# Kernel optimization log

Hardware: AMD Instinct MI355X
Metric: run time of the kernel (lower is better)

Reference implementation:

```python
import jax, jax.numpy as jnp
import numpy as np

B, N, D = 4, 256, 128
HID = 128
IN_DIM = 4 * D + 4  # h_i, h_j, |h_i-h_j|, h_i*h_j + 2 base + 2 completion feats


def setup_inputs() -> dict:
    key = jax.random.key(0)
    k1, k2, k3, k4, k5, k6, k7 = jax.random.split(key, 7)
    node_latents = jax.random.normal(k1, (B, N, D), dtype=jnp.float32)
    base_edge_logits = jax.random.normal(k2, (B, N, N), dtype=jnp.float32)
    completion_logits = jax.random.normal(k3, (B, N, N), dtype=jnp.float32)
    # MLP params (build_mlp: Linear(in,hid) -> ReLU -> Linear(hid,1) for num_layers=2)
    s1 = 1.0 / np.sqrt(IN_DIM)
    s2 = 1.0 / np.sqrt(HID)
    W1 = jax.random.uniform(k4, (IN_DIM, HID), minval=-s1, maxval=s1, dtype=jnp.float32)
    b1 = jax.random.uniform(k5, (HID,), minval=-s1, maxval=s1, dtype=jnp.float32)
    W2 = jax.random.uniform(k6, (HID, 1), minval=-s2, maxval=s2, dtype=jnp.float32)
    b2 = jax.random.uniform(k7, (1,), minval=-s2, maxval=s2, dtype=jnp.float32)
    return {"node_latents": node_latents, "base_edge_logits": base_edge_logits,
            "completion_logits": completion_logits, "W1": W1, "b1": b1, "W2": W2, "b2": b2}


def reference(node_latents, base_edge_logits, completion_logits, W1, b1, W2, b2):
    bsz, num_nodes, hidden_dim = node_latents.shape
    h_i = jnp.broadcast_to(node_latents[:, :, None, :], (bsz, num_nodes, num_nodes, hidden_dim))
    h_j = jnp.broadcast_to(node_latents[:, None, :, :], (bsz, num_nodes, num_nodes, hidden_dim))
    base = jnp.clip(base_edge_logits, -20.0, 20.0)
    comp = jnp.clip(completion_logits, -20.0, 20.0)
    pair_feat = jnp.concatenate([
        h_i, h_j, jnp.abs(h_i - h_j), h_i * h_j,
        base[..., None], jax.nn.sigmoid(base)[..., None],
        comp[..., None], jax.nn.sigmoid(comp)[..., None],
    ], axis=-1)  # [B, N, N, IN_DIM]
    hdn = jax.nn.relu(jnp.einsum('bijf,fh->bijh', pair_feat, W1) + b1)
    logits = (jnp.einsum('bijh,ho->bijo', hdn, W2) + b2)[..., 0]  # [B, N, N]
    logits = 0.5 * (logits + jnp.swapaxes(logits, 1, 2))
    diag = jnp.eye(num_nodes, dtype=bool)[None]
    return jnp.where(diag, jnp.float32(-1e9), logits)
```

## Files before the change

kernel.cpp:

```cpp
#include <hip/hip_runtime.h>
#include <cstdint>


typedef float f32x4 __attribute__((ext_vector_type(4)));

#define INV256 0.00390625f

__device__ __forceinline__ uint32_t pk4(float a, float b, float c, float d) {
  uint32_t u = __builtin_amdgcn_cvt_pk_fp8_f32(a, b, 0, false);
  u = __builtin_amdgcn_cvt_pk_fp8_f32(c, d, u, true);
  return u;
}
__device__ __forceinline__ float bf2f(unsigned short u) {
  uint32_t x = ((uint32_t)u) << 16;
  return __builtin_bit_cast(float, x);
}
__device__ __forceinline__ long mk64(uint32_t lo, uint32_t hi) {
  return (long)((((unsigned long long)hi) << 32) | lo);
}

__global__ __launch_bounds__(128) void pre_k(const float* __restrict__ node,
                                             const float* __restrict__ W1,
                                             const float* __restrict__ b1,
                                             float* __restrict__ PiB,
                                             unsigned short* __restrict__ Pjh,
                                             uint32_t* __restrict__ W1f8,
                                             float* __restrict__ out) {
  int bid = blockIdx.x;
  int tid = threadIdx.x;
  if (bid < 32) {
    int ks = bid >> 2, nip = (bid >> 1) & 1, wn = bid & 1;
    int lane = tid & 63, nilow = tid >> 6;
    int quad = lane >> 4, col = lane & 15;
    int h = wn * 64 + (nip * 2 + nilow) * 16 + col;
    int k0 = ks * 32 + quad * 8;
    float w[8];
#pragma unroll
    for (int t = 0; t < 8; ++t) w[t] = W1[(256 + k0 + t) * 128 + h] * 256.0f;
    uint2 u;
    u.x = pk4(w[0], w[1], w[2], w[3]);
    u.y = pk4(w[4], w[5], w[6], w[7]);
    reinterpret_cast<uint2*>(W1f8)[(bid * 64 + lane) * 2 + nilow] = u;
  } else if (bid < 1056) {
    __shared__ float sN[128];
    int row = bid - 32;
    int h = tid;
    sN[h] = node[row * 128 + h];
    __syncthreads();
    float ai = 0.f, aj = 0.f;
#pragma unroll 8
    for (int d = 0; d < 128; ++d) {
      float v = sN[d];
      ai = fmaf(v, W1[d * 128 + h], ai);
      aj = fmaf(v, W1[(128 + d) * 128 + h], aj);
    }
    PiB[row * 128 + h] = ai + b1[h];
    Pjh[row * 128 + h] = (unsigned short)(__builtin_bit_cast(uint32_t, aj) >> 16);
  } else {
    int r = bid - 1056;
    int i = r & 255;
    out[r * 256 + tid] = (tid == i) ? -1e9f : 0.0f;
    out[r * 256 + 128 + tid] = (tid + 128 == i) ? -1e9f : 0.0f;
  }
}

__global__ __launch_bounds__(256, 3) void main_k(
    const float* __restrict__ node, const float* __restrict__ baseL,
    const float* __restrict__ compL, const float* __restrict__ W1,
    const float* __restrict__ W2, const float* __restrict__ b2,
    const uint32_t* __restrict__ W1f8, const float* __restrict__ PiB,
    const unsigned short* __restrict__ Pjh, float* __restrict__ out) {
  __shared__ __align__(16) char smem[16640 + 32768];
  __shared__ float sHi[128];
  __shared__ float sScal[64][4];
  char* sF = smem;
  char* sB = smem + 16640;

  const int tid = threadIdx.x;
  const int bx = blockIdx.x;
  const int jt = bx & 3;
  const int i = (bx >> 2) & 255;
  const int b = bx >> 10;
  const int j0 = jt * 64;
  const int rowI = b * 256 + i;
  const int jbase = b * 256 + j0;

  const int lane = tid & 63;
  const int wave = tid >> 6;
  const int wm = wave >> 1, wn = wave & 1;
  const int col = lane & 15, quad = lane >> 4;

  uint4 g[8];
#pragma unroll
  for (int it = 0; it < 8; ++it)
    g[it] = reinterpret_cast<const uint4*>(W1f8)[it * 256 + tid];

  float pj[2][4][4];
#pragma unroll
  for (int mi = 0; mi < 2; ++mi)
#pragma unroll
    for (int r = 0; r < 4; ++r) {
      int p = wm * 32 + mi * 16 + quad * 4 + r;
      const unsigned short* row = Pjh + (size_t)(jbase + p) * 128 + wn * 64 + col;
#pragma unroll
      for (int ni = 0; ni < 4; ++ni) pj[mi][r][ni] = bf2f(row[ni * 16]);
    }

  float cCi[4], cW2[4], cB0[4], cB1[4], cB2[4], cB3[4];
#pragma unroll
  for (int ni = 0; ni < 4; ++ni) {
    int h = wn * 64 + ni * 16 + col;
    cCi[ni] = PiB[rowI * 128 + h];
    cW2[ni] = W2[h];
    cB0[ni] = W1[512 * 128 + h];
    cB1[ni] = W1[513 * 128 + h];
    cB2[ni] = W1[514 * 128 + h];
    cB3[ni] = W1[515 * 128 + h];
  }
  const float b2v = b2[0];

  if (tid < 128) sHi[tid] = node[rowI * 128 + tid];
  if (tid < 64) {
    float bl = fminf(fmaxf(baseL[rowI * 256 + j0 + tid], -20.f), 20.f);
    float cl = fminf(fmaxf(compL[rowI * 256 + j0 + tid], -20.f), 20.f);
    sScal[tid][0] = bl;
    sScal[tid][1] = 1.f / (1.f + __expf(-bl));
    sScal[tid][2] = cl;
    sScal[tid][3] = 1.f / (1.f + __expf(-cl));
  }
#pragma unroll
  for (int it = 0; it < 8; ++it)
    reinterpret_cast<uint4*>(sB)[it * 256 + tid] = g[it];
  __syncthreads();

  {
    const int d4 = tid & 31;
    const int r = tid >> 5;
    const float4 hi = *reinterpret_cast<const float4*>(&sHi[d4 * 4]);
    const int ks1 = d4 >> 3;
    const int qj = (d4 >> 1) & 3;
    const int kb = (d4 & 1) * 4;
#pragma unroll
    for (int pass = 0; pass < 8; ++pass) {
      int j = pass * 8 + r;
      const float4 hj =
          *reinterpret_cast<const float4*>(node + (size_t)(jbase + j) * 128 + d4 * 4);
      uint32_t du = pk4(fabsf(hi.x - hj.x), fabsf(hi.y - hj.y),
                        fabsf(hi.z - hj.z), fabsf(hi.w - hj.w));
      uint32_t pu = pk4(hi.x * hj.x, hi.y * hj.y, hi.z * hj.z, hi.w * hj.w);
      int colj = j & 15, m16 = j >> 4;
      int off = (m16 >> 1) * 1024 + (qj * 16 + colj) * 16 + (m16 & 1) * 8 + kb;
      *reinterpret_cast<uint32_t*>(sF + ks1 * 2080 + off) = du;
      *reinterpret_cast<uint32_t*>(sF + (4 + ks1) * 2080 + off) = pu;
    }
  }
  __syncthreads();

  f32x4 acc[2][4] = {};
#pragma unroll
  for (int ks = 0; ks < 8; ++ks) {
    uint4 b01 = *reinterpret_cast<const uint4*>(sB + ((ks * 2 + 0) * 2 + wn) * 1024 + lane * 16);
    uint4 b23 = *reinterpret_cast<const uint4*>(sB + ((ks * 2 + 1) * 2 + wn) * 1024 + lane * 16);
    uint4 aa = *reinterpret_cast<const uint4*>(sF + ks * 2080 + wm * 1024 + lane * 16);
    long a0 = mk64(aa.x, aa.y), a1 = mk64(aa.z, aa.w);
    long bb0 = mk64(b01.x, b01.y), bb1 = mk64(b01.z, b01.w);
    long bb2 = mk64(b23.x, b23.y), bb3 = mk64(b23.z, b23.w);
    acc[0][0] = __builtin_amdgcn_mfma_f32_16x16x32_fp8_fp8(a0, bb0, acc[0][0], 0, 0, 0);
    acc[0][1] = __builtin_amdgcn_mfma_f32_16x16x32_fp8_fp8(a0, bb1, acc[0][1], 0, 0, 0);
    acc[0][2] = __builtin_amdgcn_mfma_f32_16x16x32_fp8_fp8(a0, bb2, acc[0][2], 0, 0, 0);
    acc[0][3] = __builtin_amdgcn_mfma_f32_16x16x32_fp8_fp8(a0, bb3, acc[0][3], 0, 0, 0);
    acc[1][0] = __builtin_amdgcn_mfma_f32_16x16x32_fp8_fp8(a1, bb0, acc[1][0], 0, 0, 0);
    acc[1][1] = __builtin_amdgcn_mfma_f32_16x16x32_fp8_fp8(a1, bb1, acc[1][1], 0, 0, 0);
    acc[1][2] = __builtin_amdgcn_mfma_f32_16x16x32_fp8_fp8(a1, bb2, acc[1][2], 0, 0, 0);
    acc[1][3] = __builtin_amdgcn_mfma_f32_16x16x32_fp8_fp8(a1, bb3, acc[1][3], 0, 0, 0);
  }

  __syncthreads();
  float(*sPart)[33] = reinterpret_cast<float(*)[33]>(sF);

#pragma unroll
  for (int mi = 0; mi < 2; ++mi) {
#pragma unroll
    for (int r = 0; r < 4; ++r) {
      int p = wm * 32 + mi * 16 + quad * 4 + r;
      float s0 = sScal[p][0], s1 = sScal[p][1], s2 = sScal[p][2], s3 = sScal[p][3];
      float val = 0.f;
#pragma unroll
      for (int ni = 0; ni < 4; ++ni) {
        float pre = fmaf(acc[mi][ni][r], INV256, cCi[ni]) + pj[mi][r][ni];
        pre = fmaf(s0, cB0[ni], pre);
        pre = fmaf(s1, cB1[ni], pre);
        pre = fmaf(s2, cB2[ni], pre);
        pre = fmaf(s3, cB3[ni], pre);
        val = fmaf(fmaxf(pre, 0.f), cW2[ni], val);
      }
      sPart[p][wn * 16 + col] = val;
    }
  }
  __syncthreads();
  if (tid < 64) {
    float s = b2v;
#pragma unroll
    for (int c = 0; c < 32; ++c) s += sPart[tid][c];
    int jg = j0 + tid;
    if (jg != i) {
      atomicAdd(out + (size_t)(b * 256 + i) * 256 + jg, 0.5f * s);
      atomicAdd(out + (size_t)(b * 256 + jg) * 256 + i, 0.5f * s);
    }
  }
}

extern "C" void kernel_launch(void* const* d_in, const int* in_sizes, int n_in,
                              void* d_out, int out_size, void* d_ws, size_t ws_size,
                              hipStream_t stream) {
  const float* node = (const float*)d_in[0];
  const float* baseL = (const float*)d_in[1];
  const float* compL = (const float*)d_in[2];
  const float* W1 = (const float*)d_in[3];
  const float* b1 = (const float*)d_in[4];
  const float* W2 = (const float*)d_in[5];
  const float* b2 = (const float*)d_in[6];
  float* out = (float*)d_out;

  char* ws = (char*)d_ws;
  float* PiB = (float*)(ws);
  unsigned short* Pjh = (unsigned short*)(ws + (512 << 10));
  uint32_t* W1f8 = (uint32_t*)(ws + (768 << 10));

  pre_k<<<2080, 128, 0, stream>>>(node, W1, b1, PiB, Pjh, W1f8, out);
  main_k<<<4096, 256, 0, stream>>>(node, baseL, compL, W1, W2, b2, W1f8, PiB, Pjh, out);
}
```

Measured before the change: 105.3 us.

## Exploit pair symmetry: compute upper-triangular 8x8 tiles, write both orders directly

```diff
diff --git a/kernel.cpp b/kernel.cpp
--- a/kernel.cpp
+++ b/kernel.cpp
@@ -11,10 +11,6 @@
   u = __builtin_amdgcn_cvt_pk_fp8_f32(c, d, u, true);
   return u;
 }
-__device__ __forceinline__ float bf2f(unsigned short u) {
-  uint32_t x = ((uint32_t)u) << 16;
-  return __builtin_bit_cast(float, x);
-}
 __device__ __forceinline__ long mk64(uint32_t lo, uint32_t hi) {
   return (long)((((unsigned long long)hi) << 32) | lo);
 }
@@ -23,9 +19,8 @@
                                              const float* __restrict__ W1,
                                              const float* __restrict__ b1,
                                              float* __restrict__ PiB,
-                                             unsigned short* __restrict__ Pjh,
-                                             uint32_t* __restrict__ W1f8,
-                                             float* __restrict__ out) {
+                                             float* __restrict__ Pjf,
+                                             uint32_t* __restrict__ W1f8) {
   int bid = blockIdx.x;
   int tid = threadIdx.x;
   if (bid < 32) {
@@ -41,7 +36,7 @@
     u.x = pk4(w[0], w[1], w[2], w[3]);
     u.y = pk4(w[4], w[5], w[6], w[7]);
     reinterpret_cast<uint2*>(W1f8)[(bid * 64 + lane) * 2 + nilow] = u;
-  } else if (bid < 1056) {
+  } else {
     __shared__ float sN[128];
     int row = bid - 32;
     int h = tid;
@@ -55,12 +50,7 @@
       aj = fmaf(v, W1[(128 + d) * 128 + h], aj);
     }
     PiB[row * 128 + h] = ai + b1[h];
-    Pjh[row * 128 + h] = (unsigned short)(__builtin_bit_cast(uint32_t, aj) >> 16);
-  } else {
-    int r = bid - 1056;
-    int i = r & 255;
-    out[r * 256 + tid] = (tid == i) ? -1e9f : 0.0f;
-    out[r * 256 + 128 + tid] = (tid + 128 == i) ? -1e9f : 0.0f;
+    Pjf[row * 128 + h] = aj;
   }
 }
 
@@ -69,21 +59,25 @@
     const float* __restrict__ compL, const float* __restrict__ W1,
     const float* __restrict__ W2, const float* __restrict__ b2,
     const uint32_t* __restrict__ W1f8, const float* __restrict__ PiB,
-    const unsigned short* __restrict__ Pjh, float* __restrict__ out) {
+    const float* __restrict__ Pjf, float* __restrict__ out) {
   __shared__ __align__(16) char smem[16640 + 32768];
-  __shared__ float sHi[128];
-  __shared__ float sScal[64][4];
+  __shared__ float sScalF[64][4];
+  __shared__ float sScalM[64][4];
   char* sF = smem;
   char* sB = smem + 16640;
+  float* sNode = reinterpret_cast<float*>(sB);
 
   const int tid = threadIdx.x;
   const int bx = blockIdx.x;
-  const int jt = bx & 3;
-  const int i = (bx >> 2) & 255;
-  const int b = bx >> 10;
-  const int j0 = jt * 64;
-  const int rowI = b * 256 + i;
-  const int jbase = b * 256 + j0;
+  const int b = bx / 528;
+  const int t = bx - b * 528;
+  int tI = (int)((65.0f - sqrtf(4225.0f - 8.0f * (float)t)) * 0.5f);
+  tI = (tI < 0) ? 0 : (tI > 31 ? 31 : tI);
+  while (((65 * tI - tI * tI) >> 1) > t) --tI;
+  while (tI < 31 && ((65 * (tI + 1) - (tI + 1) * (tI + 1)) >> 1) <= t) ++tI;
+  const int tJ = tI + (t - ((65 * tI - tI * tI) >> 1));
+  const int I0 = tI * 8, J0 = tJ * 8;
+  const int rowB = b * 256;
 
   const int lane = tid & 63;
   const int wave = tid >> 6;
@@ -95,22 +89,33 @@
   for (int it = 0; it < 8; ++it)
     g[it] = reinterpret_cast<const uint4*>(W1f8)[it * 256 + tid];
 
-  float pj[2][4][4];
-#pragma unroll
-  for (int mi = 0; mi < 2; ++mi)
-#pragma unroll
-    for (int r = 0; r < 4; ++r) {
-      int p = wm * 32 + mi * 16 + quad * 4 + r;
-      const unsigned short* row = Pjh + (size_t)(jbase + p) * 128 + wn * 64 + col;
-#pragma unroll
-      for (int ni = 0; ni < 4; ++ni) pj[mi][r][ni] = bf2f(row[ni * 16]);
-    }
-
-  float cCi[4], cW2[4], cB0[4], cB1[4], cB2[4], cB3[4];
+#pragma unroll
+  for (int it = 0; it < 2; ++it) {
+    int idx = it * 256 + tid;
+    int row = idx >> 5, d4 = idx & 31;
+    int gr = rowB + ((row < 8) ? (I0 + row) : (J0 + row - 8));
+    reinterpret_cast<float4*>(sNode)[idx] =
+        reinterpret_cast<const float4*>(node + (size_t)gr * 128)[d4];
+  }
+
+  if (tid < 128) {
+    int p = tid & 63;
+    int mir = tid >> 6;
+    int iN = I0 + (p >> 3), jN = J0 + (p & 7);
+    int rr = mir ? jN : iN, cc = mir ? iN : jN;
+    float bl = fminf(fmaxf(baseL[(size_t)(rowB + rr) * 256 + cc], -20.f), 20.f);
+    float cl = fminf(fmaxf(compL[(size_t)(rowB + rr) * 256 + cc], -20.f), 20.f);
+    float* dst = mir ? sScalM[p] : sScalF[p];
+    dst[0] = bl;
+    dst[1] = 1.f / (1.f + __expf(-bl));
+    dst[2] = cl;
+    dst[3] = 1.f / (1.f + __expf(-cl));
+  }
+
+  float cW2[4], cB0[4], cB1[4], cB2[4], cB3[4];
 #pragma unroll
   for (int ni = 0; ni < 4; ++ni) {
     int h = wn * 64 + ni * 16 + col;
-    cCi[ni] = PiB[rowI * 128 + h];
     cW2[ni] = W2[h];
     cB0[ni] = W1[512 * 128 + h];
     cB1[ni] = W1[513 * 128 + h];
@@ -119,41 +124,51 @@
   }
   const float b2v = b2[0];
 
-  if (tid < 128) sHi[tid] = node[rowI * 128 + tid];
-  if (tid < 64) {
-    float bl = fminf(fmaxf(baseL[rowI * 256 + j0 + tid], -20.f), 20.f);
-    float cl = fminf(fmaxf(compL[rowI * 256 + j0 + tid], -20.f), 20.f);
-    sScal[tid][0] = bl;
-    sScal[tid][1] = 1.f / (1.f + __expf(-bl));
-    sScal[tid][2] = cl;
-    sScal[tid][3] = 1.f / (1.f + __expf(-cl));
-  }
-#pragma unroll
-  for (int it = 0; it < 8; ++it)
-    reinterpret_cast<uint4*>(sB)[it * 256 + tid] = g[it];
+  float piI[2][4], pjI[2][4], piJ[4][4], pjJ[4][4];
+#pragma unroll
+  for (int mi = 0; mi < 2; ++mi) {
+    int gi = rowB + I0 + wm * 4 + mi * 2 + (quad >> 1);
+#pragma unroll
+    for (int ni = 0; ni < 4; ++ni) {
+      int h = wn * 64 + ni * 16 + col;
+      piI[mi][ni] = PiB[(size_t)gi * 128 + h];
+      pjI[mi][ni] = Pjf[(size_t)gi * 128 + h];
+    }
+  }
+#pragma unroll
+  for (int r = 0; r < 4; ++r) {
+    int gj = rowB + J0 + (quad & 1) * 4 + r;
+#pragma unroll
+    for (int ni = 0; ni < 4; ++ni) {
+      int h = wn * 64 + ni * 16 + col;
+      piJ[r][ni] = PiB[(size_t)gj * 128 + h];
+      pjJ[r][ni] = Pjf[(size_t)gj * 128 + h];
+    }
+  }
   __syncthreads();
 
   {
     const int d4 = tid & 31;
-    const int r = tid >> 5;
-    const float4 hi = *reinterpret_cast<const float4*>(&sHi[d4 * 4]);
-    const int ks1 = d4 >> 3;
-    const int qj = (d4 >> 1) & 3;
-    const int kb = (d4 & 1) * 4;
+    const int rr = tid >> 5;
+    const int ks1 = d4 >> 3, qj = (d4 >> 1) & 3, kb = (d4 & 1) * 4;
+    const float4 hj = reinterpret_cast<const float4*>(sNode + (8 + rr) * 128)[d4];
 #pragma unroll
     for (int pass = 0; pass < 8; ++pass) {
-      int j = pass * 8 + r;
-      const float4 hj =
-          *reinterpret_cast<const float4*>(node + (size_t)(jbase + j) * 128 + d4 * 4);
+      const float4 hi = reinterpret_cast<const float4*>(sNode + pass * 128)[d4];
       uint32_t du = pk4(fabsf(hi.x - hj.x), fabsf(hi.y - hj.y),
                         fabsf(hi.z - hj.z), fabsf(hi.w - hj.w));
       uint32_t pu = pk4(hi.x * hj.x, hi.y * hj.y, hi.z * hj.z, hi.w * hj.w);
-      int colj = j & 15, m16 = j >> 4;
+      int p = pass * 8 + rr;
+      int colj = p & 15, m16 = p >> 4;
       int off = (m16 >> 1) * 1024 + (qj * 16 + colj) * 16 + (m16 & 1) * 8 + kb;
       *reinterpret_cast<uint32_t*>(sF + ks1 * 2080 + off) = du;
       *reinterpret_cast<uint32_t*>(sF + (4 + ks1) * 2080 + off) = pu;
     }
   }
+  __syncthreads();
+#pragma unroll
+  for (int it = 0; it < 8; ++it)
+    reinterpret_cast<uint4*>(sB)[it * 256 + tid] = g[it];
   __syncthreads();
 
   f32x4 acc[2][4] = {};
@@ -176,36 +191,53 @@
   }
 
   __syncthreads();
-  float(*sPart)[33] = reinterpret_cast<float(*)[33]>(sF);
+  float(*sPF)[33] = reinterpret_cast<float(*)[33]>(smem);
+  float(*sPM)[33] = reinterpret_cast<float(*)[33]>(smem + 16640);
 
 #pragma unroll
   for (int mi = 0; mi < 2; ++mi) {
 #pragma unroll
     for (int r = 0; r < 4; ++r) {
       int p = wm * 32 + mi * 16 + quad * 4 + r;
-      float s0 = sScal[p][0], s1 = sScal[p][1], s2 = sScal[p][2], s3 = sScal[p][3];
-      float val = 0.f;
+      float f0 = sScalF[p][0], f1 = sScalF[p][1], f2 = sScalF[p][2], f3 = sScalF[p][3];
+      float m0 = sScalM[p][0], m1 = sScalM[p][1], m2 = sScalM[p][2], m3 = sScalM[p][3];
+      float vf = 0.f, vm = 0.f;
 #pragma unroll
       for (int ni = 0; ni < 4; ++ni) {
-        float pre = fmaf(acc[mi][ni][r], INV256, cCi[ni]) + pj[mi][r][ni];
-        pre = fmaf(s0, cB0[ni], pre);
-        pre = fmaf(s1, cB1[ni], pre);
-        pre = fmaf(s2, cB2[ni], pre);
-        pre = fmaf(s3, cB3[ni], pre);
-        val = fmaf(fmaxf(pre, 0.f), cW2[ni], val);
+        float gv = acc[mi][ni][r] * INV256;
+        float pf = (gv + piI[mi][ni]) + pjJ[r][ni];
+        pf = fmaf(f0, cB0[ni], pf);
+        pf = fmaf(f1, cB1[ni], pf);
+        pf = fmaf(f2, cB2[ni], pf);
+        pf = fmaf(f3, cB3[ni], pf);
+        float pm = (gv + piJ[r][ni]) + pjI[mi][ni];
+        pm = fmaf(m0, cB0[ni], pm);
+        pm = fmaf(m1, cB1[ni], pm);
+        pm = fmaf(m2, cB2[ni], pm);
+        pm = fmaf(m3, cB3[ni], pm);
+        vf = fmaf(fmaxf(pf, 0.f), cW2[ni], vf);
+        vm = fmaf(fmaxf(pm, 0.f), cW2[ni], vm);
       }
-      sPart[p][wn * 16 + col] = val;
+      sPF[p][wn * 16 + col] = vf;
+      sPM[p][wn * 16 + col] = vm;
     }
   }
   __syncthreads();
   if (tid < 64) {
-    float s = b2v;
-#pragma unroll
-    for (int c = 0; c < 32; ++c) s += sPart[tid][c];
-    int jg = j0 + tid;
-    if (jg != i) {
-      atomicAdd(out + (size_t)(b * 256 + i) * 256 + jg, 0.5f * s);
-      atomicAdd(out + (size_t)(b * 256 + jg) * 256 + i, 0.5f * s);
+    int p = tid;
+    float sumF = 0.f, sumM = 0.f;
+#pragma unroll
+    for (int c = 0; c < 32; ++c) {
+      sumF += sPF[p][c];
+      sumM += sPM[p][c];
+    }
+    float val = 0.5f * (sumF + sumM) + b2v;
+    int iN = I0 + (p >> 3), jN = J0 + (p & 7);
+    if (iN == jN) {
+      out[(size_t)(rowB + iN) * 256 + jN] = -1e9f;
+    } else {
+      out[(size_t)(rowB + iN) * 256 + jN] = val;
+      out[(size_t)(rowB + jN) * 256 + iN] = val;
     }
   }
 }
@@ -224,9 +256,9 @@
 
   char* ws = (char*)d_ws;
   float* PiB = (float*)(ws);
-  unsigned short* Pjh = (unsigned short*)(ws + (512 << 10));
-  uint32_t* W1f8 = (uint32_t*)(ws + (768 << 10));
-
-  pre_k<<<2080, 128, 0, stream>>>(node, W1, b1, PiB, Pjh, W1f8, out);
-  main_k<<<4096, 256, 0, stream>>>(node, baseL, compL, W1, W2, b2, W1f8, PiB, Pjh, out);
-}
+  float* Pjf = (float*)(ws + (512 << 10));
+  uint32_t* W1f8 = (uint32_t*)(ws + (1024 << 10));
+
+  pre_k<<<1056, 128, 0, stream>>>(node, W1, b1, PiB, Pjf, W1f8);
+  main_k<<<2112, 256, 0, stream>>>(node, baseL, compL, W1, W2, b2, W1f8, PiB, Pjf, out);
+}
```

Result: slower. 108.0 us (+2.6%).
